# Kernel tuning notes

Measured on AMD Instinct MI355X. Metric: run time of the kernel, lower is better.

Reference implementation:

```python
import jax, jax.numpy as jnp
import numpy as np

NUM_TYPES = 4
IN_DIM = 128
HID_DIM = 256
OUT_DIM = 128
NUM_NODES = 100000


def setup_inputs() -> dict:
    key = jax.random.key(0)
    k_x, k_t, k_w1, k_b1, k_w2, k_b2 = jax.random.split(key, 6)
    raw_features = jax.random.normal(k_x, (NUM_NODES, IN_DIM), dtype=jnp.float32)
    node_type = jax.random.randint(k_t, (NUM_NODES,), 0, NUM_TYPES, dtype=jnp.int64)
    # stacked per-type MLP params (Kaiming-ish scale like torch Linear defaults)
    W1 = jax.random.uniform(k_w1, (NUM_TYPES, IN_DIM, HID_DIM), dtype=jnp.float32,
                            minval=-1.0, maxval=1.0) / np.sqrt(IN_DIM)
    b1 = jax.random.uniform(k_b1, (NUM_TYPES, HID_DIM), dtype=jnp.float32,
                            minval=-1.0, maxval=1.0) / np.sqrt(IN_DIM)
    W2 = jax.random.uniform(k_w2, (NUM_TYPES, HID_DIM, OUT_DIM), dtype=jnp.float32,
                            minval=-1.0, maxval=1.0) / np.sqrt(HID_DIM)
    b2 = jax.random.uniform(k_b2, (NUM_TYPES, OUT_DIM), dtype=jnp.float32,
                            minval=-1.0, maxval=1.0) / np.sqrt(HID_DIM)
    return {"raw_features": raw_features, "node_type": node_type,
            "W1": W1, "b1": b1, "W2": W2, "b2": b2}


def reference(raw_features, node_type, W1, b1, W2, b2):
    # Run every expert on every node (num_types is tiny), then select per node.
    # h: [types, nodes, hidden]
    h = jax.nn.relu(jnp.einsum('ni,tih->tnh', raw_features, W1) + b1[:, None, :])
    # out_all: [types, nodes, out]
    out_all = jnp.einsum('tnh,tho->tno', h, W2) + b2[:, None, :]
    # select expert output matching each node's type -> [nodes, out]
    encoded = out_all[node_type, jnp.arange(raw_features.shape[0])]
    return encoded
```

## Files before the change

### kernel.cpp

```cpp
#include <hip/hip_runtime.h>
#include <hip/hip_bf16.h>

typedef float f32x4 __attribute__((ext_vector_type(4)));
typedef short short8 __attribute__((ext_vector_type(8)));

#define NTYPES 4


static __device__ __forceinline__ unsigned short f2bf(float f) {
  union { float f; unsigned int u; } v; v.f = f;
  unsigned int u = v.u;
  unsigned int r = u + 0x7FFFu + ((u >> 16) & 1u);
  return (unsigned short)(r >> 16);
}

static __device__ __forceinline__ unsigned int pkbf(float a, float b) {
  __hip_bfloat162 h = __float22bfloat162_rn(make_float2(a, b));
  union { __hip_bfloat162 h; unsigned int u; } v; v.h = h;
  return v.u;
}

static __device__ __forceinline__ void prep_tile(int role, int tid,
    const float* __restrict__ W1, const float* __restrict__ W2,
    unsigned short* __restrict__ W1T, unsigned short* __restrict__ W2T,
    unsigned short (*sp)[72]) {
  const int bb = role & 31;
  const int tt = bb >> 3, ti = bb & 7;
  const float* src; unsigned short* dst; int scols, tr, tc;
  if (role < 32) { src = W1 + tt * 32768; dst = W1T + tt * 32768; scols = 256; tr = ti >> 2; tc = ti & 3; }
  else           { src = W2 + tt * 32768; dst = W2T + tt * 32768; scols = 128; tr = ti >> 1; tc = ti & 1; }
  const int srows = 32768 / scols;
  const int r0 = tid >> 4, cw = (tid & 15) << 2;
  #pragma unroll
  for (int i = 0; i < 4; ++i) {
    int r = tr * 64 + i * 16 + r0;
    float4 v = *(const float4*)(src + r * scols + tc * 64 + cw);
    sp[i * 16 + r0][cw + 0] = f2bf(v.x);
    sp[i * 16 + r0][cw + 1] = f2bf(v.y);
    sp[i * 16 + r0][cw + 2] = f2bf(v.z);
    sp[i * 16 + r0][cw + 3] = f2bf(v.w);
  }
  __syncthreads();
  #pragma unroll
  for (int i = 0; i < 4; ++i) {
    int orow = i * 16 + r0;
    ushort4 u;
    u.x = sp[cw + 0][orow];
    u.y = sp[cw + 1][orow];
    u.z = sp[cw + 2][orow];
    u.w = sp[cw + 3][orow];
    *(ushort4*)(dst + (tc * 64 + orow) * srows + tr * 64 + cw) = u;
  }
}

static __device__ __forceinline__ void mlp_body(
    int t, int lb, int nblk, int g0, int g1, int tid,
    const float* __restrict__ X, const int* __restrict__ perm,
    const unsigned short* __restrict__ W1T, const unsigned short* __restrict__ W2T,
    const float* __restrict__ B1, const float* __restrict__ B2,
    float* __restrict__ OUT, float* __restrict__ dump,
    unsigned char* x_lds, unsigned char* h_lds, int (*s_rid)[64]) {
  const int l  = tid & 63, w = tid >> 6;
  const int lo = l & 15,  hi = l >> 4;
  const int nt2 = g1 - g0 - lb;
  if (nt2 <= 0) return;
  const int cnt = (nt2 + nblk - 1) / nblk;

  const int rg = tid >> 5;
  const int c4 = (tid & 31) * 4;

  if (tid < 64) s_rid[0][tid] = perm[(g0 + lb) * 64 + tid];
  __syncthreads();
  float4 xv[8];
  #pragma unroll
  for (int p = 0; p < 8; ++p) {
    int rd = s_rid[0][p * 8 + rg];
    xv[p] = make_float4(0.f, 0.f, 0.f, 0.f);
    if (rd >= 0) xv[p] = *(const float4*)(X + (size_t)rd * 128 + c4);
  }

  const unsigned short* w1t = W1T + (t << 15);
  const unsigned short* w2t = W2T + (t << 15);
  short8 a1[4][4];
  #pragma unroll
  for (int ks = 0; ks < 4; ++ks)
    #pragma unroll
    for (int m = 0; m < 4; ++m)
      a1[ks][m] = *(const short8*)(w1t + (w * 64 + m * 16 + lo) * 128 + ks * 32 + hi * 8);
  short8 a2[8][2];
  #pragma unroll
  for (int ks = 0; ks < 8; ++ks)
    #pragma unroll
    for (int mo = 0; mo < 2; ++mo)
      a2[ks][mo] = *(const short8*)(w2t + (w * 32 + mo * 16 + lo) * 256 + ks * 32 + hi * 8);
  f32x4 bb1[4], bb2[2];
  #pragma unroll
  for (int m = 0; m < 4; ++m)
    bb1[m] = *(const f32x4*)(B1 + t * 256 + w * 64 + m * 16 + hi * 4);
  #pragma unroll
  for (int mo = 0; mo < 2; ++mo)
    bb2[mo] = *(const f32x4*)(B2 + t * 128 + w * 32 + mo * 16 + hi * 4);

  for (int j = 0; j < cnt; ++j) {
    const int g = g0 + lb + j * nblk;
    const bool hn = (j + 1 < cnt);
    const int cur = j & 1, nxt = cur ^ 1;

    #pragma unroll
    for (int p = 0; p < 8; ++p) {
      int row = p * 8 + rg;
      uint2 u;
      u.x = pkbf(xv[p].x, xv[p].y);
      u.y = pkbf(xv[p].z, xv[p].w);
      int byte = (row * 256 + c4 * 2) ^ ((row & 7) << 4);
      *(uint2*)(x_lds + byte) = u;
    }
    __syncthreads();

    if (hn && tid < 64) s_rid[nxt][tid] = perm[(g + nblk) * 64 + tid];

    f32x4 acc[4][4];
    #pragma unroll
    for (int m = 0; m < 4; ++m)
      #pragma unroll
      for (int n2 = 0; n2 < 4; ++n2) acc[m][n2] = (f32x4){0.f, 0.f, 0.f, 0.f};
    #pragma unroll
    for (int ks = 0; ks < 4; ++ks) {
      short8 b[4];
      #pragma unroll
      for (int n2 = 0; n2 < 4; ++n2) {
        int row = n2 * 16 + lo;
        int byte = (row * 256 + ks * 64 + hi * 16) ^ ((row & 7) << 4);
        b[n2] = *(const short8*)(x_lds + byte);
      }
      #pragma unroll
      for (int m = 0; m < 4; ++m)
        #pragma unroll
        for (int n2 = 0; n2 < 4; ++n2)
          acc[m][n2] = __builtin_amdgcn_mfma_f32_16x16x32_bf16(a1[ks][m], b[n2], acc[m][n2], 0, 0, 0);
    }

    #pragma unroll
    for (int m = 0; m < 4; ++m) {
      const int hw2 = w * 128 + m * 32 + hi * 8;
      #pragma unroll
      for (int n2 = 0; n2 < 4; ++n2) {
        int node = n2 * 16 + lo;
        uint2 hu;
        hu.x = pkbf(fmaxf(acc[m][n2][0] + bb1[m][0], 0.f),
                    fmaxf(acc[m][n2][1] + bb1[m][1], 0.f));
        hu.y = pkbf(fmaxf(acc[m][n2][2] + bb1[m][2], 0.f),
                    fmaxf(acc[m][n2][3] + bb1[m][3], 0.f));
        int byte = (node * 512 + hw2) ^ ((node & 7) << 4);
        *(uint2*)(h_lds + byte) = hu;
      }
    }
    __syncthreads();

    float4 nv[8];
    #pragma unroll
    for (int p = 0; p < 8; ++p) nv[p] = make_float4(0.f, 0.f, 0.f, 0.f);
    if (hn) {
      #pragma unroll
      for (int p = 0; p < 8; ++p) {
        int rd = s_rid[nxt][p * 8 + rg];
        if (rd >= 0) nv[p] = *(const float4*)(X + (size_t)rd * 128 + c4);
      }
    }

    f32x4 acc2[2][4];
    #pragma unroll
    for (int mo = 0; mo < 2; ++mo)
      #pragma unroll
      for (int n2 = 0; n2 < 4; ++n2) acc2[mo][n2] = (f32x4){0.f, 0.f, 0.f, 0.f};
    #pragma unroll
    for (int ks = 0; ks < 8; ++ks) {
      short8 b[4];
      #pragma unroll
      for (int n2 = 0; n2 < 4; ++n2) {
        int node = n2 * 16 + lo;
        int byte = (node * 512 + ks * 64 + hi * 16) ^ ((node & 7) << 4);
        b[n2] = *(const short8*)(h_lds + byte);
      }
      #pragma unroll
      for (int mo = 0; mo < 2; ++mo)
        #pragma unroll
        for (int n2 = 0; n2 < 4; ++n2)
          acc2[mo][n2] = __builtin_amdgcn_mfma_f32_16x16x32_bf16(a2[ks][mo], b[n2], acc2[mo][n2], 0, 0, 0);
    }
    __syncthreads();

    #pragma unroll
    for (int mo = 0; mo < 2; ++mo) {
      const int oc = w * 32 + mo * 16 + hi * 4;
      #pragma unroll
      for (int n2 = 0; n2 < 4; ++n2) {
        int node = n2 * 16 + lo;
        f32x4 o = acc2[mo][n2];
        o[0] += bb2[mo][0]; o[1] += bb2[mo][1];
        o[2] += bb2[mo][2]; o[3] += bb2[mo][3];
        int byte = (node * 512 + oc * 4) ^ ((node & 7) << 4);
        *(f32x4*)(h_lds + byte) = o;
      }
    }
    __syncthreads();

    #pragma unroll
    for (int p = 0; p < 8; ++p) {
      int row = p * 8 + rg;
      int rd = s_rid[cur][row];
      f32x4 v = *(const f32x4*)(h_lds + ((row * 512 + c4 * 4) ^ ((row & 7) << 4)));
      float* dst = (rd >= 0) ? (OUT + (size_t)rd * 128 + c4) : (dump + c4);
      *(f32x4*)dst = v;
    }

    #pragma unroll
    for (int p = 0; p < 8; ++p) xv[p] = nv[p];
  }
}

__global__ __launch_bounds__(256) void k_hp(
    const float* __restrict__ W1, const float* __restrict__ W2,
    unsigned short* __restrict__ W1T, unsigned short* __restrict__ W2T,
    const int* __restrict__ NT, int n, int* __restrict__ cnts) {
  __shared__ unsigned short sp[64][72];
  __shared__ int lc[NTYPES];
  const int tid = threadIdx.x;
  if (blockIdx.x < 64) {
    prep_tile(blockIdx.x, tid, W1, W2, W1T, W2T, sp);
  } else {
    int hb = blockIdx.x - 64;
    if (tid < NTYPES) lc[tid] = 0;
    __syncthreads();
    int i = hb * 256 + tid;
    if (i < n) atomicAdd(&lc[NT[i]], 1);
    __syncthreads();
    if (tid < NTYPES) cnts[hb * NTYPES + tid] = lc[tid];
  }
}

__global__ __launch_bounds__(256) void k_scatter2(
    const int* __restrict__ NT, int n, const int* __restrict__ cnts, int nbH,
    int* __restrict__ perm, int* __restrict__ bases) {
  __shared__ int s_tot[NTYPES], s_pre[NTYPES], lc[NTYPES];
  const int tid = threadIdx.x;
  const int bid = blockIdx.x;
  const int l = tid & 63, w = tid >> 6;
  {
    int tot = 0, pre = 0;
    for (int b = l; b < nbH; b += 64) {
      int c = cnts[b * NTYPES + w];
      tot += c;
      pre += (b < bid) ? c : 0;
    }
    #pragma unroll
    for (int off = 32; off; off >>= 1) {
      tot += __shfl_down(tot, off);
      pre += __shfl_down(pre, off);
    }
    if (l == 0) { s_tot[w] = tot; s_pre[w] = pre; }
  }
  __syncthreads();
  int sb[NTYPES + 1];
  sb[0] = 0;
  #pragma unroll
  for (int tau = 0; tau < NTYPES; ++tau)
    sb[tau + 1] = sb[tau] + ((s_tot[tau] + 63) & ~63);
  if (bid == 0 && tid <= NTYPES) bases[tid] = sb[tid];
  if (tid < NTYPES) lc[tid] = 0;
  __syncthreads();
  int i = bid * 256 + tid;
  if (i < n) {
    int tt = NT[i];
    int r = atomicAdd(&lc[tt], 1);
    perm[sb[tt] + s_pre[tt] + r] = i;
  }
  if (bid < NTYPES) {
    for (int p = sb[bid] + s_tot[bid] + tid; p < sb[bid + 1]; p += 256)
      perm[p] = -1;
  }
}

__global__ __launch_bounds__(256, 1) void k_mlpw_fb(
    const float* __restrict__ X, const int* __restrict__ perm,
    const int* __restrict__ bases,
    const unsigned short* __restrict__ W1T, const unsigned short* __restrict__ W2T,
    const float* __restrict__ B1, const float* __restrict__ B2,
    float* __restrict__ OUT, float* __restrict__ dump) {
  __shared__ __align__(16) unsigned char x_lds[16384];
  __shared__ __align__(16) unsigned char h_lds[32768];
  __shared__ int s_rid[2][64];
  const int t = blockIdx.x >> 7, lb = blockIdx.x & 127;
  mlp_body(t, lb, 128, bases[t] >> 6, bases[t + 1] >> 6, threadIdx.x,
           X, perm, W1T, W2T, B1, B2, OUT, dump, x_lds, h_lds, s_rid);
}

extern "C" void kernel_launch(void* const* d_in, const int* in_sizes, int n_in,
                              void* d_out, int out_size, void* d_ws, size_t ws_size,
                              hipStream_t stream) {
  const float* X  = (const float*)d_in[0];
  const int*   NT = (const int*)d_in[1];
  const float* W1 = (const float*)d_in[2];
  const float* B1 = (const float*)d_in[3];
  const float* W2 = (const float*)d_in[4];
  const float* B2 = (const float*)d_in[5];
  float* OUT = (float*)d_out;
  int n = in_sizes[1];

  char* ws = (char*)d_ws;
  float* dump = (float*)(ws + 512);
  int* bases = (int*)(ws + 2048);
  int* cnts = (int*)(ws + 4096);
  int* perm = (int*)(ws + 16384);
  unsigned short* W1T = (unsigned short*)(ws + 524288);
  unsigned short* W2T = (unsigned short*)(ws + 786432);

  const int nbH = (n + 255) / 256;
  k_hp<<<64 + nbH, 256, 0, stream>>>(W1, W2, W1T, W2T, NT, n, cnts);
  k_scatter2<<<nbH, 256, 0, stream>>>(NT, n, cnts, nbH, perm, bases);
  k_mlpw_fb<<<512, 256, 0, stream>>>(X, perm, bases, W1T, W2T, B1, B2, OUT, dump);
}
```

Baseline: 49.31 us.

## Replace global type sort with per-block local bucketing in fused MLP

Drops the global histogram and scatter kernels and the persistent per-type MLP kernel. Each block of 256 nodes now sorts its own nodes by type in shared memory, then runs 64-node sub-tiles where every type present in a sub-tile executes its MLP only on the 16-row fragments it covers. This removes two launches and the global permutation round trip. In exchange, weights are reloaded from global memory per sub-tile and per type rather than kept resident in registers. Fragments that straddle type boundaries also compute redundant MFMAs, and about 391 blocks run at one block per CU, so some CUs may be underused.

New measurement: 138.4 us. 181% more time.

```diff
diff --git a/kernel.cpp b/kernel.cpp
--- a/kernel.cpp
+++ b/kernel.cpp
@@ -20,10 +20,12 @@
   return v.u;
 }
 
-static __device__ __forceinline__ void prep_tile(int role, int tid,
+__global__ __launch_bounds__(256) void k_wprep(
     const float* __restrict__ W1, const float* __restrict__ W2,
-    unsigned short* __restrict__ W1T, unsigned short* __restrict__ W2T,
-    unsigned short (*sp)[72]) {
+    unsigned short* __restrict__ W1T, unsigned short* __restrict__ W2T) {
+  __shared__ unsigned short sp[64][72];
+  const int tid = threadIdx.x;
+  const int role = blockIdx.x;
   const int bb = role & 31;
   const int tt = bb >> 3, ti = bb & 7;
   const float* src; unsigned short* dst; int scols, tr, tc;
@@ -53,246 +55,182 @@
   }
 }
 
-static __device__ __forceinline__ void mlp_body(
-    int t, int lb, int nblk, int g0, int g1, int tid,
-    const float* __restrict__ X, const int* __restrict__ perm,
+__global__ __launch_bounds__(256, 1) void k_mlpn(
+    const float* __restrict__ X, const int* __restrict__ NT,
     const unsigned short* __restrict__ W1T, const unsigned short* __restrict__ W2T,
     const float* __restrict__ B1, const float* __restrict__ B2,
-    float* __restrict__ OUT, float* __restrict__ dump,
-    unsigned char* x_lds, unsigned char* h_lds, int (*s_rid)[64]) {
+    float* __restrict__ OUT, int n) {
+  __shared__ __align__(16) unsigned char x_lds[16384];
+  __shared__ __align__(16) unsigned char h_lds[32768];
+  __shared__ int s_nat[256];
+  __shared__ unsigned char s_ty[256];
+  __shared__ int s_hist[NTYPES];
+  __shared__ int s_pb[NTYPES + 1];
+
+  const int tid = threadIdx.x;
+  const int nb = blockIdx.x * 256;
+
+  if (tid < NTYPES) s_hist[tid] = 0;
+  __syncthreads();
+  const int g = nb + tid;
+  int ty = NTYPES - 1;
+  if (g < n) ty = NT[g];
+  int r = atomicAdd(&s_hist[ty], 1);
+  __syncthreads();
+  if (tid == 0) {
+    int b = 0;
+    s_pb[0] = 0;
+    for (int t = 0; t < NTYPES; ++t) { b += s_hist[t]; s_pb[t + 1] = b; }
+  }
+  __syncthreads();
+  {
+    int p = s_pb[ty] + r;
+    s_nat[p] = tid;
+    s_ty[p] = (unsigned char)ty;
+  }
+  __syncthreads();
+
   const int l  = tid & 63, w = tid >> 6;
   const int lo = l & 15,  hi = l >> 4;
-  const int nt2 = g1 - g0 - lb;
-  if (nt2 <= 0) return;
-  const int cnt = (nt2 + nblk - 1) / nblk;
-
   const int rg = tid >> 5;
   const int c4 = (tid & 31) * 4;
 
-  if (tid < 64) s_rid[0][tid] = perm[(g0 + lb) * 64 + tid];
-  __syncthreads();
-  float4 xv[8];
-  #pragma unroll
-  for (int p = 0; p < 8; ++p) {
-    int rd = s_rid[0][p * 8 + rg];
-    xv[p] = make_float4(0.f, 0.f, 0.f, 0.f);
-    if (rd >= 0) xv[p] = *(const float4*)(X + (size_t)rd * 128 + c4);
-  }
-
-  const unsigned short* w1t = W1T + (t << 15);
-  const unsigned short* w2t = W2T + (t << 15);
-  short8 a1[4][4];
-  #pragma unroll
-  for (int ks = 0; ks < 4; ++ks)
+  for (int s = 0; s < 4; ++s) {
+    const int base = s * 64;
+
     #pragma unroll
-    for (int m = 0; m < 4; ++m)
-      a1[ks][m] = *(const short8*)(w1t + (w * 64 + m * 16 + lo) * 128 + ks * 32 + hi * 8);
-  short8 a2[8][2];
-  #pragma unroll
-  for (int ks = 0; ks < 8; ++ks)
-    #pragma unroll
-    for (int mo = 0; mo < 2; ++mo)
-      a2[ks][mo] = *(const short8*)(w2t + (w * 32 + mo * 16 + lo) * 256 + ks * 32 + hi * 8);
-  f32x4 bb1[4], bb2[2];
-  #pragma unroll
-  for (int m = 0; m < 4; ++m)
-    bb1[m] = *(const f32x4*)(B1 + t * 256 + w * 64 + m * 16 + hi * 4);
-  #pragma unroll
-  for (int mo = 0; mo < 2; ++mo)
-    bb2[mo] = *(const f32x4*)(B2 + t * 128 + w * 32 + mo * 16 + hi * 4);
-
-  for (int j = 0; j < cnt; ++j) {
-    const int g = g0 + lb + j * nblk;
-    const bool hn = (j + 1 < cnt);
-    const int cur = j & 1, nxt = cur ^ 1;
-
-    #pragma unroll
-    for (int p = 0; p < 8; ++p) {
-      int row = p * 8 + rg;
+    for (int q = 0; q < 8; ++q) {
+      int row = q * 8 + rg;
+      int gg = nb + s_nat[base + row];
+      float4 v = make_float4(0.f, 0.f, 0.f, 0.f);
+      if (gg < n) v = *(const float4*)(X + (size_t)gg * 128 + c4);
       uint2 u;
-      u.x = pkbf(xv[p].x, xv[p].y);
-      u.y = pkbf(xv[p].z, xv[p].w);
+      u.x = pkbf(v.x, v.y);
+      u.y = pkbf(v.z, v.w);
       int byte = (row * 256 + c4 * 2) ^ ((row & 7) << 4);
       *(uint2*)(x_lds + byte) = u;
     }
     __syncthreads();
 
-    if (hn && tid < 64) s_rid[nxt][tid] = perm[(g + nblk) * 64 + tid];
-
-    f32x4 acc[4][4];
-    #pragma unroll
-    for (int m = 0; m < 4; ++m)
-      #pragma unroll
-      for (int n2 = 0; n2 < 4; ++n2) acc[m][n2] = (f32x4){0.f, 0.f, 0.f, 0.f};
-    #pragma unroll
-    for (int ks = 0; ks < 4; ++ks) {
-      short8 b[4];
-      #pragma unroll
-      for (int n2 = 0; n2 < 4; ++n2) {
-        int row = n2 * 16 + lo;
-        int byte = (row * 256 + ks * 64 + hi * 16) ^ ((row & 7) << 4);
-        b[n2] = *(const short8*)(x_lds + byte);
-      }
+    for (int t = 0; t < NTYPES; ++t) {
+      const int lo_p = s_pb[t] - base;
+      const int hi_p = s_pb[t + 1] - base;
+      if (hi_p <= 0 || lo_p >= 64) continue;
+      const int flo = max(0, lo_p) >> 4;
+      const int fhi = (min(64, hi_p) - 1) >> 4;
+
+      const unsigned short* w1t = W1T + (t << 15);
+      short8 a1t[4][4];
+      #pragma unroll
+      for (int ks = 0; ks < 4; ++ks)
+        #pragma unroll
+        for (int m = 0; m < 4; ++m)
+          a1t[ks][m] = *(const short8*)(w1t + (w * 64 + m * 16 + lo) * 128 + ks * 32 + hi * 8);
+
+      f32x4 acc[4][4];
       #pragma unroll
       for (int m = 0; m < 4; ++m)
         #pragma unroll
-        for (int n2 = 0; n2 < 4; ++n2)
-          acc[m][n2] = __builtin_amdgcn_mfma_f32_16x16x32_bf16(a1[ks][m], b[n2], acc[m][n2], 0, 0, 0);
-    }
-
-    #pragma unroll
-    for (int m = 0; m < 4; ++m) {
-      const int hw2 = w * 128 + m * 32 + hi * 8;
-      #pragma unroll
-      for (int n2 = 0; n2 < 4; ++n2) {
-        int node = n2 * 16 + lo;
-        uint2 hu;
-        hu.x = pkbf(fmaxf(acc[m][n2][0] + bb1[m][0], 0.f),
-                    fmaxf(acc[m][n2][1] + bb1[m][1], 0.f));
-        hu.y = pkbf(fmaxf(acc[m][n2][2] + bb1[m][2], 0.f),
-                    fmaxf(acc[m][n2][3] + bb1[m][3], 0.f));
-        int byte = (node * 512 + hw2) ^ ((node & 7) << 4);
-        *(uint2*)(h_lds + byte) = hu;
+        for (int nf = 0; nf < 4; ++nf) acc[m][nf] = (f32x4){0.f, 0.f, 0.f, 0.f};
+      #pragma unroll
+      for (int ks = 0; ks < 4; ++ks) {
+        short8 b[4];
+        #pragma unroll
+        for (int nf = 0; nf < 4; ++nf) {
+          if (nf < flo || nf > fhi) continue;
+          int row = nf * 16 + lo;
+          int byte = (row * 256 + ks * 64 + hi * 16) ^ ((row & 7) << 4);
+          b[nf] = *(const short8*)(x_lds + byte);
+        }
+        #pragma unroll
+        for (int m = 0; m < 4; ++m)
+          #pragma unroll
+          for (int nf = 0; nf < 4; ++nf) {
+            if (nf < flo || nf > fhi) continue;
+            acc[m][nf] = __builtin_amdgcn_mfma_f32_16x16x32_bf16(a1t[ks][m], b[nf], acc[m][nf], 0, 0, 0);
+          }
+      }
+
+      #pragma unroll
+      for (int m = 0; m < 4; ++m) {
+        f32x4 bb = *(const f32x4*)(B1 + t * 256 + w * 64 + m * 16 + hi * 4);
+        const int hw2 = w * 128 + m * 32 + hi * 8;
+        #pragma unroll
+        for (int nf = 0; nf < 4; ++nf) {
+          if (nf < flo || nf > fhi) continue;
+          int row = nf * 16 + lo;
+          if (s_ty[base + row] == (unsigned char)t) {
+            uint2 hu;
+            hu.x = pkbf(fmaxf(acc[m][nf][0] + bb[0], 0.f),
+                        fmaxf(acc[m][nf][1] + bb[1], 0.f));
+            hu.y = pkbf(fmaxf(acc[m][nf][2] + bb[2], 0.f),
+                        fmaxf(acc[m][nf][3] + bb[3], 0.f));
+            int byte = (row * 512 + hw2) ^ ((row & 7) << 4);
+            *(uint2*)(h_lds + byte) = hu;
+          }
+        }
       }
     }
     __syncthreads();
 
-    float4 nv[8];
-    #pragma unroll
-    for (int p = 0; p < 8; ++p) nv[p] = make_float4(0.f, 0.f, 0.f, 0.f);
-    if (hn) {
-      #pragma unroll
-      for (int p = 0; p < 8; ++p) {
-        int rd = s_rid[nxt][p * 8 + rg];
-        if (rd >= 0) nv[p] = *(const float4*)(X + (size_t)rd * 128 + c4);
-      }
-    }
-
-    f32x4 acc2[2][4];
-    #pragma unroll
-    for (int mo = 0; mo < 2; ++mo)
-      #pragma unroll
-      for (int n2 = 0; n2 < 4; ++n2) acc2[mo][n2] = (f32x4){0.f, 0.f, 0.f, 0.f};
-    #pragma unroll
-    for (int ks = 0; ks < 8; ++ks) {
-      short8 b[4];
-      #pragma unroll
-      for (int n2 = 0; n2 < 4; ++n2) {
-        int node = n2 * 16 + lo;
-        int byte = (node * 512 + ks * 64 + hi * 16) ^ ((node & 7) << 4);
-        b[n2] = *(const short8*)(h_lds + byte);
-      }
+    for (int t = 0; t < NTYPES; ++t) {
+      const int lo_p = s_pb[t] - base;
+      const int hi_p = s_pb[t + 1] - base;
+      if (hi_p <= 0 || lo_p >= 64) continue;
+      const int flo = max(0, lo_p) >> 4;
+      const int fhi = (min(64, hi_p) - 1) >> 4;
+
+      const unsigned short* w2t = W2T + (t << 15);
+      short8 a2t[8][2];
+      #pragma unroll
+      for (int ks = 0; ks < 8; ++ks)
+        #pragma unroll
+        for (int mo = 0; mo < 2; ++mo)
+          a2t[ks][mo] = *(const short8*)(w2t + (w * 32 + mo * 16 + lo) * 256 + ks * 32 + hi * 8);
+
+      f32x4 acc2[2][4];
       #pragma unroll
       for (int mo = 0; mo < 2; ++mo)
         #pragma unroll
-        for (int n2 = 0; n2 < 4; ++n2)
-          acc2[mo][n2] = __builtin_amdgcn_mfma_f32_16x16x32_bf16(a2[ks][mo], b[n2], acc2[mo][n2], 0, 0, 0);
+        for (int nf = 0; nf < 4; ++nf) acc2[mo][nf] = (f32x4){0.f, 0.f, 0.f, 0.f};
+      #pragma unroll
+      for (int ks = 0; ks < 8; ++ks) {
+        short8 b[4];
+        #pragma unroll
+        for (int nf = 0; nf < 4; ++nf) {
+          if (nf < flo || nf > fhi) continue;
+          int row = nf * 16 + lo;
+          int byte = (row * 512 + ks * 64 + hi * 16) ^ ((row & 7) << 4);
+          b[nf] = *(const short8*)(h_lds + byte);
+        }
+        #pragma unroll
+        for (int mo = 0; mo < 2; ++mo)
+          #pragma unroll
+          for (int nf = 0; nf < 4; ++nf) {
+            if (nf < flo || nf > fhi) continue;
+            acc2[mo][nf] = __builtin_amdgcn_mfma_f32_16x16x32_bf16(a2t[ks][mo], b[nf], acc2[mo][nf], 0, 0, 0);
+          }
+      }
+
+      #pragma unroll
+      for (int mo = 0; mo < 2; ++mo) {
+        f32x4 bb = *(const f32x4*)(B2 + t * 128 + w * 32 + mo * 16 + hi * 4);
+        const int oc = w * 32 + mo * 16 + hi * 4;
+        #pragma unroll
+        for (int nf = 0; nf < 4; ++nf) {
+          if (nf < flo || nf > fhi) continue;
+          int row = nf * 16 + lo;
+          int gg = nb + s_nat[base + row];
+          if (s_ty[base + row] == (unsigned char)t && gg < n) {
+            f32x4 o = acc2[mo][nf];
+            o[0] += bb[0]; o[1] += bb[1]; o[2] += bb[2]; o[3] += bb[3];
+            *(f32x4*)(OUT + (size_t)gg * 128 + oc) = o;
+          }
+        }
+      }
     }
     __syncthreads();
-
-    #pragma unroll
-    for (int mo = 0; mo < 2; ++mo) {
-      const int oc = w * 32 + mo * 16 + hi * 4;
-      #pragma unroll
-      for (int n2 = 0; n2 < 4; ++n2) {
-        int node = n2 * 16 + lo;
-        f32x4 o = acc2[mo][n2];
-        o[0] += bb2[mo][0]; o[1] += bb2[mo][1];
-        o[2] += bb2[mo][2]; o[3] += bb2[mo][3];
-        int byte = (node * 512 + oc * 4) ^ ((node & 7) << 4);
-        *(f32x4*)(h_lds + byte) = o;
-      }
-    }
-    __syncthreads();
-
-    #pragma unroll
-    for (int p = 0; p < 8; ++p) {
-      int row = p * 8 + rg;
-      int rd = s_rid[cur][row];
-      f32x4 v = *(const f32x4*)(h_lds + ((row * 512 + c4 * 4) ^ ((row & 7) << 4)));
-      float* dst = (rd >= 0) ? (OUT + (size_t)rd * 128 + c4) : (dump + c4);
-      *(f32x4*)dst = v;
-    }
-
-    #pragma unroll
-    for (int p = 0; p < 8; ++p) xv[p] = nv[p];
-  }
-}
-
-__global__ __launch_bounds__(256) void k_hp(
-    const float* __restrict__ W1, const float* __restrict__ W2,
-    unsigned short* __restrict__ W1T, unsigned short* __restrict__ W2T,
-    const int* __restrict__ NT, int n, int* __restrict__ cnts) {
-  __shared__ unsigned short sp[64][72];
-  __shared__ int lc[NTYPES];
-  const int tid = threadIdx.x;
-  if (blockIdx.x < 64) {
-    prep_tile(blockIdx.x, tid, W1, W2, W1T, W2T, sp);
-  } else {
-    int hb = blockIdx.x - 64;
-    if (tid < NTYPES) lc[tid] = 0;
-    __syncthreads();
-    int i = hb * 256 + tid;
-    if (i < n) atomicAdd(&lc[NT[i]], 1);
-    __syncthreads();
-    if (tid < NTYPES) cnts[hb * NTYPES + tid] = lc[tid];
-  }
-}
-
-__global__ __launch_bounds__(256) void k_scatter2(
-    const int* __restrict__ NT, int n, const int* __restrict__ cnts, int nbH,
-    int* __restrict__ perm, int* __restrict__ bases) {
-  __shared__ int s_tot[NTYPES], s_pre[NTYPES], lc[NTYPES];
-  const int tid = threadIdx.x;
-  const int bid = blockIdx.x;
-  const int l = tid & 63, w = tid >> 6;
-  {
-    int tot = 0, pre = 0;
-    for (int b = l; b < nbH; b += 64) {
-      int c = cnts[b * NTYPES + w];
-      tot += c;
-      pre += (b < bid) ? c : 0;
-    }
-    #pragma unroll
-    for (int off = 32; off; off >>= 1) {
-      tot += __shfl_down(tot, off);
-      pre += __shfl_down(pre, off);
-    }
-    if (l == 0) { s_tot[w] = tot; s_pre[w] = pre; }
-  }
-  __syncthreads();
-  int sb[NTYPES + 1];
-  sb[0] = 0;
-  #pragma unroll
-  for (int tau = 0; tau < NTYPES; ++tau)
-    sb[tau + 1] = sb[tau] + ((s_tot[tau] + 63) & ~63);
-  if (bid == 0 && tid <= NTYPES) bases[tid] = sb[tid];
-  if (tid < NTYPES) lc[tid] = 0;
-  __syncthreads();
-  int i = bid * 256 + tid;
-  if (i < n) {
-    int tt = NT[i];
-    int r = atomicAdd(&lc[tt], 1);
-    perm[sb[tt] + s_pre[tt] + r] = i;
-  }
-  if (bid < NTYPES) {
-    for (int p = sb[bid] + s_tot[bid] + tid; p < sb[bid + 1]; p += 256)
-      perm[p] = -1;
-  }
-}
-
-__global__ __launch_bounds__(256, 1) void k_mlpw_fb(
-    const float* __restrict__ X, const int* __restrict__ perm,
-    const int* __restrict__ bases,
-    const unsigned short* __restrict__ W1T, const unsigned short* __restrict__ W2T,
-    const float* __restrict__ B1, const float* __restrict__ B2,
-    float* __restrict__ OUT, float* __restrict__ dump) {
-  __shared__ __align__(16) unsigned char x_lds[16384];
-  __shared__ __align__(16) unsigned char h_lds[32768];
-  __shared__ int s_rid[2][64];
-  const int t = blockIdx.x >> 7, lb = blockIdx.x & 127;
-  mlp_body(t, lb, 128, bases[t] >> 6, bases[t + 1] >> 6, threadIdx.x,
-           X, perm, W1T, W2T, B1, B2, OUT, dump, x_lds, h_lds, s_rid);
+  }
 }
 
 extern "C" void kernel_launch(void* const* d_in, const int* in_sizes, int n_in,
@@ -308,15 +246,10 @@
   int n = in_sizes[1];
 
   char* ws = (char*)d_ws;
-  float* dump = (float*)(ws + 512);
-  int* bases = (int*)(ws + 2048);
-  int* cnts = (int*)(ws + 4096);
-  int* perm = (int*)(ws + 16384);
   unsigned short* W1T = (unsigned short*)(ws + 524288);
   unsigned short* W2T = (unsigned short*)(ws + 786432);
 
-  const int nbH = (n + 255) / 256;
-  k_hp<<<64 + nbH, 256, 0, stream>>>(W1, W2, W1T, W2T, NT, n, cnts);
-  k_scatter2<<<nbH, 256, 0, stream>>>(NT, n, cnts, nbH, perm, bases);
-  k_mlpw_fb<<<512, 256, 0, stream>>>(X, perm, bases, W1T, W2T, B1, B2, OUT, dump);
-}
+  k_wprep<<<64, 256, 0, stream>>>(W1, W2, W1T, W2T);
+  const int nblk = (n + 255) / 256;
+  k_mlpn<<<nblk, 256, 0, stream>>>(X, NT, W1T, W2T, B1, B2, OUT, n);
+}
```
